# Kernel optimization log

Hardware: AMD Instinct MI355X
Metric: run time of the kernel (lower is better)

The kernel has to match this reference:

```python
import jax, jax.numpy as jnp
import numpy as np

B, EMBED, H, W = 2, 32, 96, 96
SQ = (4, 2); R = 2; EXP = 2
SCH = EMBED // SQ[0]            # 8  squeezed channel dim
SHSP = SCH * R * R              # 32 shuffled spatial dim
SSP = SHSP // SQ[1]             # 16 squeezed spatial dim (attention embed dim)
HEADS = SCH * EXP               # 16
EACH = SSP // SCH               # 2
IDX = np.array([i + j * SCH for i in range(SCH) for j in range(EACH)])
NIDX = np.array([i + j * EACH for i in range(EACH) for j in range(SCH)])


def conv(x, w, b, stride=1, pad=0, groups=1):
    y = jax.lax.conv_general_dilated(x, w, (stride, stride), [(pad, pad), (pad, pad)],
                                     feature_group_count=groups,
                                     dimension_numbers=('NCHW', 'OIHW', 'NCHW'))
    return y + b[None, :, None, None]


def ln_ch(x, w, b):
    # LayerNorm over channel dim (torch applies it on [B,HW,C])
    mu = x.mean(1, keepdims=True)
    var = ((x - mu) ** 2).mean(1, keepdims=True)
    return (x - mu) * jax.lax.rsqrt(var + 1e-5) * w[None, :, None, None] + b[None, :, None, None]


def l2n(x, axis):
    # F.normalize: divide by L2 norm clamped to eps
    return x / jnp.maximum(jnp.sqrt(jnp.sum(x * x, axis=axis, keepdims=True)), 1e-12)


def _qkv(x, wqkv, bqkv):
    Bb, C, Hh, Ww = x.shape
    qkv = conv(x, wqkv, bqkv, groups=C)                        # [B, C*EXP*3, H, W], per-channel 1x1
    qkv = qkv.reshape(Bb, C, EXP * 3, Hh, Ww).transpose(0, 2, 1, 3, 4)
    q, k, v = jnp.split(qkv, 3, axis=1)                        # each [B, EXP, C, H, W]
    hd = EXP * C // HEADS
    rs = lambda a: a.reshape(Bb, HEADS, hd, Hh * Ww)
    return rs(q), rs(k), rs(v)


def _fuse(o, wfus, bfus, Bb, C, Hh, Ww):
    o = o.reshape(Bb, EXP, C, Hh, Ww).transpose(0, 2, 1, 3, 4).reshape(Bb, C * EXP, Hh, Ww)
    return conv(o, wfus, bfus, groups=C)


def chan_attn(x, wqkv, bqkv, t, wfus, bfus):
    Bb, C, Hh, Ww = x.shape
    q, k, v = _qkv(x, wqkv, bqkv)
    q, k = l2n(q, -1), l2n(k, -1)
    a = jax.nn.softmax(jnp.einsum('bhdn,bhen->bhde', q, k) * t, axis=-1)   # [B,h,d,d]
    o = jnp.einsum('bhde,bhen->bhdn', a, v)
    return _fuse(o, wfus, bfus, Bb, C, Hh, Ww)


def spat_attn(x, wqkv, bqkv, t, wfus, bfus):
    Bb, C, Hh, Ww = x.shape
    q, k, v = _qkv(x, wqkv, bqkv)
    q, k = l2n(q, -2), l2n(k, -2)
    a = jax.nn.softmax(jnp.einsum('bhdn,bhdm->bhnm', q, k) * t, axis=-1)   # [B,h,HW,HW]
    o = jnp.einsum('bhnm,bhdm->bhdn', a, v)
    return _fuse(o, wfus, bfus, Bb, C, Hh, Ww)


def pixel_shuffle(x, r):
    Bb, C, Hh, Ww = x.shape
    x = x.reshape(Bb, C // (r * r), r, r, Hh, Ww).transpose(0, 1, 4, 2, 5, 3)
    return x.reshape(Bb, C // (r * r), Hh * r, Ww * r)


def _forward(x, ln1_w, ln1_b, cab_w1, cab_b1, cab_w2, cab_b2, cab_aw1, cab_ab1, cab_aw2, cab_ab2,
             sq1_w, sq1_b, sq2_w, sq2_b, ca_qkv_w, ca_qkv_b, ca_t, ca_fus_w, ca_fus_b,
             sa_qkv_w, sa_qkv_b, sa_t, sa_fus_w, sa_fus_b, un1_w, un1_b, un2_w, un2_b,
             ln2_w, ln2_b, da_w1, da_b1, da_dw_w, da_dw_b, da_pw, da_pb):
    Bb, C, Hh, Ww = x.shape
    xn = ln_ch(x, ln1_w, ln1_b)
    # ---- CAB branch (conv-GELU-conv + RCAN channel attention) ----
    c = jax.nn.gelu(conv(xn, cab_w1, cab_b1, pad=1), approximate=False)
    c = conv(c, cab_w2, cab_b2, pad=1)
    y = c.mean((2, 3), keepdims=True)
    y = jax.nn.relu(conv(y, cab_aw1, cab_ab1))
    y = jax.nn.sigmoid(conv(y, cab_aw2, cab_ab2))
    x_cab = c * y
    # ---- Condensed attention branch ----
    z = conv(xn, sq1_w, sq1_b)                                   # 1x1: C -> SCH
    z = conv(z, sq2_w, sq2_b, stride=R, groups=SCH)              # grouped RxR stride R: -> [B,SSP,H/R,W/R]
    z = z[:, IDX]
    z = chan_attn(z, ca_qkv_w, ca_qkv_b, ca_t, ca_fus_w, ca_fus_b)
    z = z[:, NIDX]
    z = spat_attn(z, sa_qkv_w, sa_qkv_b, sa_t, sa_fus_w, sa_fus_b)
    z = conv(z, un1_w, un1_b, groups=SCH)                        # SSP -> SHSP
    z = pixel_shuffle(z, R)                                      # -> [B,SCH,H,W]
    z = conv(z, un2_w, un2_b)                                    # SCH -> C
    x = x + z + x_cab
    # ---- Dual adaptive (gated depthwise-conv FFN) ----
    xn2 = ln_ch(x, ln2_w, ln2_b)
    d = conv(xn2, da_w1, da_b1)
    d = conv(d, da_dw_w, da_dw_b, pad=3, groups=C).reshape(Bb, C, 2, Hh, Ww)
    d = jax.nn.gelu(d[:, :, 0], approximate=False) * jax.nn.sigmoid(d[:, :, 1])
    d = conv(d, da_pw, da_pb)
    return x + d


def setup_inputs():
    key = jax.random.key(0)
    ks = iter(jax.random.split(key, 40))
    nrm = lambda s: jax.random.normal(next(ks), s, jnp.float32) * 0.05
    inp = {'x': jax.random.normal(next(ks), (B, EMBED, H, W), jnp.float32)}
    wshapes = {
        'cab_w1': (EMBED // 4, EMBED, 3, 3), 'cab_w2': (EMBED, EMBED // 4, 3, 3),
        'cab_aw1': (EMBED // 18, EMBED, 1, 1), 'cab_aw2': (EMBED, EMBED // 18, 1, 1),
        'sq1_w': (SCH, EMBED, 1, 1), 'sq2_w': (SSP, 1, R, R),
        'ca_qkv_w': (SSP * EXP * 3, 1, 1, 1), 'ca_fus_w': (SSP, EXP, 1, 1),
        'sa_qkv_w': (SSP * EXP * 3, 1, 1, 1), 'sa_fus_w': (SSP, EXP, 1, 1),
        'un1_w': (SHSP, SSP // SCH, 1, 1), 'un2_w': (EMBED, SCH, 1, 1),
        'da_w1': (EMBED, EMBED, 1, 1), 'da_dw_w': (2 * EMBED, 1, 7, 7), 'da_pw': (EMBED, EMBED, 1, 1),
    }
    bshapes = {'cab_b1': EMBED // 4, 'cab_b2': EMBED, 'cab_ab1': EMBED // 18, 'cab_ab2': EMBED,
               'sq1_b': SCH, 'sq2_b': SSP, 'ca_qkv_b': SSP * EXP * 3, 'ca_fus_b': SSP,
               'sa_qkv_b': SSP * EXP * 3, 'sa_fus_b': SSP, 'un1_b': SHSP, 'un2_b': EMBED,
               'da_b1': EMBED, 'da_dw_b': 2 * EMBED, 'da_pb': EMBED}
    for n, s in wshapes.items():
        inp[n] = nrm(s)
    for n, s in bshapes.items():
        inp[n] = nrm((s,))
    inp['ln1_w'] = jnp.ones((EMBED,), jnp.float32); inp['ln1_b'] = jnp.zeros((EMBED,), jnp.float32)
    inp['ln2_w'] = jnp.ones((EMBED,), jnp.float32); inp['ln2_b'] = jnp.zeros((EMBED,), jnp.float32)
    inp['ca_t'] = jnp.ones((1, HEADS, 1, 1), jnp.float32)
    inp['sa_t'] = jnp.ones((1, HEADS, 1, 1), jnp.float32)
    return inp


def reference(x, ln1_w, ln1_b, cab_w1, cab_b1, cab_w2, cab_b2, cab_aw1, cab_ab1, cab_aw2, cab_ab2,
              sq1_w, sq1_b, sq2_w, sq2_b, ca_qkv_w, ca_qkv_b, ca_t, ca_fus_w, ca_fus_b,
              sa_qkv_w, sa_qkv_b, sa_t, sa_fus_w, sa_fus_b, un1_w, un1_b, un2_w, un2_b,
              ln2_w, ln2_b, da_w1, da_b1, da_dw_w, da_dw_b, da_pw, da_pb):
    return _forward(x, ln1_w, ln1_b, cab_w1, cab_b1, cab_w2, cab_b2, cab_aw1, cab_ab1, cab_aw2, cab_ab2,
                    sq1_w, sq1_b, sq2_w, sq2_b, ca_qkv_w, ca_qkv_b, ca_t, ca_fus_w, ca_fus_b,
                    sa_qkv_w, sa_qkv_b, sa_t, sa_fus_w, sa_fus_b, un1_w, un1_b, un2_w, un2_b,
                    ln2_w, ln2_b, da_w1, da_b1, da_dw_w, da_dw_b, da_pw, da_pb)
```

## Files before the change

### kernel.cpp

```cpp
#include <hip/hip_runtime.h>
#include <cstdint>
#include <math.h>

#define NP 9216
#define NP2 2304
#define KH 12
#define NMOM 78

__device__ __forceinline__ float gelu_ex(float v){
  return 0.5f*v*(1.0f+erff(v*0.70710678118654752440f));
}
__device__ __forceinline__ float sigm(float v){
  return 1.0f/(1.0f+__expf(-v));
}

__global__ __launch_bounds__(256) void k_ln1(const float* __restrict__ x,
    const float* __restrict__ lw, const float* __restrict__ lb,
    const float* __restrict__ sw, const float* __restrict__ sb,
    float* __restrict__ xn, float* __restrict__ z1)
{
  __shared__ float sred[2][8][32];
  __shared__ float xnsh[32][33];
  int p = threadIdx.x & 31, sl = threadIdx.x >> 5;
  int pix = blockIdx.x*32 + p;
  int b = pix / NP, n = pix % NP;
  const float* xp = x + (size_t)b*32*NP + (size_t)(sl*4)*NP + n;
  float v[4]; float s=0.f, s2=0.f;
#pragma unroll
  for (int c=0;c<4;c++){ float t=xp[(size_t)c*NP]; v[c]=t; s+=t; s2+=t*t; }
  sred[0][sl][p]=s; sred[1][sl][p]=s2;
  __syncthreads();
  s=0.f; s2=0.f;
#pragma unroll
  for (int g=0;g<8;g++){ s += sred[0][g][p]; s2 += sred[1][g][p]; }
  float mu = s*(1.f/32.f);
  float var = s2*(1.f/32.f)-mu*mu;
  float rs = rsqrtf(var+1e-5f);
  float* xo = xn + (size_t)b*32*NP + (size_t)(sl*4)*NP + n;
#pragma unroll
  for (int c=0;c<4;c++){
    int cc = sl*4+c;
    float t = (v[c]-mu)*rs*lw[cc]+lb[cc];
    xo[(size_t)c*NP] = t;
    xnsh[p][cc] = t;
  }
  __syncthreads();
  float vv[32];
#pragma unroll
  for (int c=0;c<32;c++) vv[c]=xnsh[p][c];
  int g = sl;
  float a = sb[g];
#pragma unroll
  for (int c=0;c<32;c++) a += vv[c]*sw[g*32+c];
  z1[(size_t)b*8*NP + (size_t)g*NP + n] = a;
}

__global__ __launch_bounds__(256) void k_phB(const float* __restrict__ xn,
    const float* __restrict__ w1, const float* __restrict__ b1,
    const float* __restrict__ z1, const float* __restrict__ w2,
    const float* __restrict__ b2,
    float* __restrict__ c1, float* __restrict__ u, float* __restrict__ spart)
{
  if (blockIdx.x < 576){
    int og = blockIdx.x/72, pb = blockIdx.x%72;
    int idx = pb*256+threadIdx.x;
    int b = idx/NP, n = idx%NP, i = n/96, j = n%96;
    float acc = b1[og];
    const float* xb = xn + (size_t)b*32*NP;
    const float* wb = w1 + og*288;
#pragma unroll
    for (int di=0;di<3;di++){
      int ii=i+di-1; if ((unsigned)ii>=96u) continue;
#pragma unroll
      for (int dj=0;dj<3;dj++){
        int jj=j+dj-1; if ((unsigned)jj>=96u) continue;
        const float* xp = xb + ii*96+jj;
        const float* wp = wb + di*3+dj;
#pragma unroll
        for (int c=0;c<32;c++) acc += xp[(size_t)c*NP]*wp[c*9];
      }
    }
    c1[(size_t)b*8*NP + (size_t)og*NP + n] = gelu_ex(acc);
  } else {
    __shared__ float red[4][5];
    int u2 = blockIdx.x-576;
    int pr = u2/18, pb = u2%18;
    int idx = pb*256+threadIdx.x;
    int b = idx/NP2, n = idx%NP2, i = n/48, j = n%48;
    int ocA = pr, ocB = pr+8;
    int gA = ocA>>1, gB = ocB>>1;
    const float* zpA = z1 + ((size_t)b*8+gA)*NP + (size_t)(2*i)*96 + 2*j;
    const float* zpB = z1 + ((size_t)b*8+gB)*NP + (size_t)(2*i)*96 + 2*j;
    float vA = zpA[0]*w2[ocA*4]+zpA[1]*w2[ocA*4+1]+zpA[96]*w2[ocA*4+2]+zpA[97]*w2[ocA*4+3]+b2[ocA];
    float vB = zpB[0]*w2[ocB*4]+zpB[1]*w2[ocB*4+1]+zpB[96]*w2[ocB*4+2]+zpB[97]*w2[ocB*4+3]+b2[ocB];
    u[((size_t)b*16+2*pr)*NP2 + n]   = vA;
    u[((size_t)b*16+2*pr+1)*NP2 + n] = vB;
    int wv=threadIdx.x>>6, ln=threadIdx.x&63;
    float st[5]={vA,vB,vA*vA,vB*vB,vA*vB};
#pragma unroll
    for (int k=0;k<5;k++){
      float r=st[k];
#pragma unroll
      for (int m=1;m<64;m<<=1) r+=__shfl_xor(r,m,64);
      if (ln==0) red[wv][k]=r;
    }
    __syncthreads();
    if (threadIdx.x<5){
      float r = red[0][threadIdx.x]+red[1][threadIdx.x]+red[2][threadIdx.x]+red[3][threadIdx.x];
      spart[(b*9 + (pb%9))*40 + pr*5 + threadIdx.x] = r;
    }
  }
}

__global__ __launch_bounds__(256) void k_phC(const float* __restrict__ c1,
    const float* __restrict__ w2, const float* __restrict__ b2,
    float* __restrict__ cbuf, float* __restrict__ ypart,
    const float* __restrict__ u, const float* __restrict__ spart,
    const float* __restrict__ cqw, const float* __restrict__ cqb,
    const float* __restrict__ cat, const float* __restrict__ cfw,
    const float* __restrict__ cfb,
    const float* __restrict__ qw, const float* __restrict__ qb,
    float2* __restrict__ qarr, float* __restrict__ mompart)
{
  if (blockIdx.x < 576){
    __shared__ float red[4][4];
    int og = blockIdx.x/72, pb = blockIdx.x%72;
    int idx = pb*256+threadIdx.x;
    int b = idx/NP, n = idx%NP, i = n/96, j = n%96;
    float acc[4];
#pragma unroll
    for (int k=0;k<4;k++) acc[k]=b2[og*4+k];
    const float* cb = c1 + (size_t)b*8*NP;
#pragma unroll
    for (int di=0;di<3;di++){
      int ii=i+di-1; if ((unsigned)ii>=96u) continue;
#pragma unroll
      for (int dj=0;dj<3;dj++){
        int jj=j+dj-1; if ((unsigned)jj>=96u) continue;
        const float* xp = cb + ii*96+jj;
#pragma unroll
        for (int c=0;c<8;c++){
          float val = xp[(size_t)c*NP];
          const float* wp = w2 + (og*4)*72 + c*9+di*3+dj;
#pragma unroll
          for (int k=0;k<4;k++) acc[k] += val*wp[k*72];
        }
      }
    }
    int wv = threadIdx.x>>6, ln = threadIdx.x&63;
#pragma unroll
    for (int k=0;k<4;k++){
      cbuf[(size_t)b*32*NP + (size_t)(og*4+k)*NP + n] = acc[k];
      float r = acc[k];
#pragma unroll
      for (int m=1;m<64;m<<=1) r += __shfl_xor(r, m, 64);
      if (ln==0) red[wv][k]=r;
    }
    __syncthreads();
    if (threadIdx.x<4){
      float r = red[0][threadIdx.x]+red[1][threadIdx.x]+red[2][threadIdx.x]+red[3][threadIdx.x];
      ypart[(og*72+pb)*4 + threadIdx.x] = r;
    }
  } else {
    __shared__ float red16[16][80];
    int u2 = blockIdx.x-576;
    int bh = u2/9, ch = u2%9;
    int n = ch*256 + threadIdx.x;
    int b = bh>>4, h = bh&15;
    int p = h&7, s = h>>3;
    int cc0=2*p, cc1=2*p+1;
    int oc0 = 2*(cc0&7)+(cc0>>3);
    int oc1 = 2*(cc1&7)+(cc1>>3);
    float AA[2], BB[2], CCc[2];
#pragma unroll
    for (int t2=0;t2<2;t2++){
      int oc = t2? oc1:oc0;
      int p2 = oc>>1, dd = oc&1;
      float st[5]={0,0,0,0,0};
      for (int ib=0; ib<9; ib++){
#pragma unroll
        for (int k=0;k<5;k++) st[k] += spart[(b*9+ib)*40 + p2*5 + k];
      }
      float S0=st[0],S1=st[1],Q00=st[2],Q11=st[3],Q01=st[4];
      float Sd = dd? S1:S0;
      float Qdd = dd? Q11:Q00;
      float cu0[2],cu1[2],ccst[2];
#pragma unroll
      for (int hh=0;hh<2;hh++){
        int h2=p2+8*hh;
        float th2=cat[h2];
        float aq=cqw[(2*p2+dd)*6+hh], bq=cqb[(2*p2+dd)*6+hh];
        float nq=fmaxf(sqrtf(fmaxf(aq*aq*Qdd+2.f*aq*bq*Sd+2304.f*bq*bq,0.f)),1e-12f);
        float m2[2],av[2],bv[2];
#pragma unroll
        for (int e=0;e<2;e++){
          float Se_=e?S1:S0, Qee=e?Q11:Q00, Qde=(dd==e)?Qdd:Q01;
          float ak=cqw[(2*p2+e)*6+2+hh], bk=cqb[(2*p2+e)*6+2+hh];
          float nk=fmaxf(sqrtf(fmaxf(ak*ak*Qee+2.f*ak*bk*Se_+2304.f*bk*bk,0.f)),1e-12f);
          float D=aq*ak*Qde + aq*bk*Sd + bq*ak*Se_ + 2304.f*bq*bk;
          m2[e]=th2*D/(nq*nk);
          av[e]=cqw[(2*p2+e)*6+4+hh]; bv[e]=cqb[(2*p2+e)*6+4+hh];
        }
        float mx=fmaxf(m2[0],m2[1]);
        float e0=__expf(m2[0]-mx), e1=__expf(m2[1]-mx);
        float inv=1.f/(e0+e1);
        cu0[hh]=e0*inv*av[0]; cu1[hh]=e1*inv*av[1]; ccst[hh]=e0*inv*bv[0]+e1*inv*bv[1];
      }
      float f0=cfw[oc*2], f1=cfw[oc*2+1];
      AA[t2]=f0*cu0[0]+f1*cu0[1];
      BB[t2]=f0*cu1[0]+f1*cu1[1];
      CCc[t2]=f0*ccst[0]+f1*ccst[1]+cfb[oc];
    }
    const float* u00 = u + ((size_t)b*16 + (oc0>>1)*2)*NP2;
    const float* u01 = u00 + NP2;
    const float* u10 = u + ((size_t)b*16 + (oc1>>1)*2)*NP2;
    const float* u11 = u10 + NP2;
    float w0 = AA[0]*u00[n]+BB[0]*u01[n]+CCc[0];
    float w1 = AA[1]*u10[n]+BB[1]*u11[n]+CCc[1];
    float k0 = qw[cc0*6+2+s]*w0+qb[cc0*6+2+s];
    float k1 = qw[cc1*6+2+s]*w1+qb[cc1*6+2+s];
    float rnk = 1.f/fmaxf(sqrtf(k0*k0+k1*k1),1e-12f);
    float kc = k0*rnk, ks = k1*rnk;
    float q0 = qw[cc0*6+s]*w0+qb[cc0*6+s];
    float q1 = qw[cc1*6+s]*w1+qb[cc1*6+s];
    float rnq = 1.f/fmaxf(sqrtf(q0*q0+q1*q1),1e-12f);
    qarr[bh*NP2+n] = make_float2(q0*rnq, q1*rnq);

    int grp = threadIdx.x>>4, gl = threadIdx.x&15;
    float c = 1.f, sn = 0.f;
#pragma unroll
    for (int k=0;k<=KH;k++){
      float vals[6] = {c, sn, c*w0, sn*w0, c*w1, sn*w1};
#pragma unroll
      for (int jv=0;jv<6;jv++){
        float r = vals[jv];
        r += __shfl_xor(r, 1, 64);
        r += __shfl_xor(r, 2, 64);
        r += __shfl_xor(r, 4, 64);
        r += __shfl_xor(r, 8, 64);
        if (gl==0) red16[grp][k*6+jv] = r;
      }
      float cn = c*kc - sn*ks;
      sn = sn*kc + c*ks;
      c = cn;
    }
    __syncthreads();
    if (threadIdx.x < NMOM){
      float r = 0.f;
#pragma unroll
      for (int g=0;g<16;g++) r += red16[g][threadIdx.x];
      mompart[(bh*9+ch)*NMOM + threadIdx.x] = r;
    }
  }
}

__global__ __launch_bounds__(256) void k_un2(
    const float* __restrict__ mompart, const float2* __restrict__ qarr,
    const float* __restrict__ sat,
    const float* __restrict__ qw, const float* __restrict__ qb,
    const float* __restrict__ fw, const float* __restrict__ fb,
    const float* __restrict__ u1w, const float* __restrict__ u1b,
    const float* __restrict__ ypart,
    const float* __restrict__ aw1, const float* __restrict__ ab1,
    const float* __restrict__ aw2, const float* __restrict__ ab2,
    const float* __restrict__ u2w, const float* __restrict__ u2b,
    const float* __restrict__ x, const float* __restrict__ cbuf,
    const float* __restrict__ lw, const float* __restrict__ lb,
    const float* __restrict__ dw1, const float* __restrict__ db1,
    float* __restrict__ xsum, float* __restrict__ d1)
{
  __shared__ float msh[16][80];
  __shared__ float fsh[16][13];
  __shared__ float sred[2][8][32];
  __shared__ float xsh[32][33];
  __shared__ float y2sh[32];
  int p = threadIdx.x & 31, sl = threadIdx.x >> 5;
  int pix = blockIdx.x*32 + p;
  int b = pix/NP, n = pix%NP;
  int tid = threadIdx.x;
  if (tid < 208){
    int h = tid/13, k = tid%13;
    double t = (double)sat[h];
    double fac;
    if (fabs(t) < 1e-3){
      double xh = 0.5*t;
      double pk = 1.0;
      for (int q=1;q<=k;q++) pk *= xh/(double)q;
      double Ik = pk*(1.0 + xh*xh/(double)(k+1));
      fac = (k? 2.0:1.0)*Ik;
    } else {
      const int KS = 36;
      double ip1 = 0.0, ik = 1e-280, sum2 = 0.0;
      double vk = 0.0, v0 = 0.0;
      for (int q=KS; q>=1; --q){
        if (q == k) vk = ik;
        sum2 += ik;
        double im1 = ip1 + (2.0*(double)q/t)*ik;
        ip1 = ik; ik = im1;
      }
      v0 = ik;
      if (k == 0) vk = v0;
      double total = v0 + 2.0*sum2;
      double scale = exp(t)/total;
      fac = (k? 2.0:1.0)*vk*scale;
    }
    fsh[h][k] = (float)fac;
  }
  for (int e = tid; e < 16*NMOM; e += 256){
    int bh = e/NMOM, jj = e%NMOM;
    float ssum = 0.f;
    for (int ib=0; ib<9; ib++)
      ssum += mompart[((size_t)(b*16+bh)*9+ib)*NMOM + jj];
    msh[bh][jj] = ssum;
  }
  if (tid < 32){
    int c = tid;
    float ssum = 0.f;
    for (int ib=0; ib<36; ib++)
      ssum += ypart[((c>>2)*72 + b*36 + ib)*4 + (c&3)];
    float pr = ssum*(1.f/9216.f)*aw1[c];
#pragma unroll
    for (int m=1;m<32;m<<=1) pr += __shfl_xor(pr, m, 64);
    float y1 = fmaxf(pr+ab1[0], 0.f);
    y2sh[c] = sigm(aw2[c]*y1+ab2[c]);
  }
  __syncthreads();
  for (int e = tid; e < 16*NMOM; e += 256){
    int bh = e/NMOM, jj = e%NMOM;
    msh[bh][jj] *= fsh[bh][jj/6];
  }
  __syncthreads();
  int ii = n/96, jj96 = n%96;
  int n48 = (ii>>1)*48 + (jj96>>1);
  int kq = (ii&1)*2 + (jj96&1);
  float pg[8];
#pragma unroll
  for (int g=0;g<8;g++){
    float o[2][2];
#pragma unroll
    for (int hh=0;hh<2;hh++){
      int h = g+8*hh;
      float2 q = qarr[(size_t)(b*16+h)*NP2 + n48];
      float c = 1.f, sn = 0.f;
      float Se=0.f, S0=0.f, S1=0.f;
#pragma unroll
      for (int k=0;k<=KH;k++){
        const float* mk = &msh[h][k*6];
        Se += c*mk[0] + sn*mk[1];
        S0 += c*mk[2] + sn*mk[3];
        S1 += c*mk[4] + sn*mk[5];
        float cn = c*q.x - sn*q.y;
        sn = sn*q.x + c*q.y;
        c = cn;
      }
      float rSe = 1.f/Se;
      float av0=qw[(2*g)*6+4+hh],  bv0=qb[(2*g)*6+4+hh];
      float av1=qw[(2*g+1)*6+4+hh],bv1=qb[(2*g+1)*6+4+hh];
      o[hh][0]=av0*S0*rSe+bv0;
      o[hh][1]=av1*S1*rSe+bv1;
    }
    float zz0 = o[0][0]*fw[(2*g)*2]   + o[1][0]*fw[(2*g)*2+1]   + fb[2*g];
    float zz1 = o[0][1]*fw[(2*g+1)*2] + o[1][1]*fw[(2*g+1)*2+1] + fb[2*g+1];
    int od = 4*g+kq;
    pg[g] = zz0*u1w[od*2] + zz1*u1w[od*2+1] + u1b[od];
  }
  float xv[4]; float s=0.f,s2=0.f;
#pragma unroll
  for (int c=0;c<4;c++){
    int cc = sl*4+c;
    float a=u2b[cc];
#pragma unroll
    for (int g=0;g<8;g++) a+=pg[g]*u2w[cc*8+g];
    size_t off=((size_t)b*32+cc)*NP+n;
    float t = x[off]+a+cbuf[off]*y2sh[cc];
    xv[c]=t; xsum[off]=t; s+=t; s2+=t*t;
  }
  sred[0][sl][p]=s; sred[1][sl][p]=s2;
  __syncthreads();
  s=0.f; s2=0.f;
#pragma unroll
  for (int g=0;g<8;g++){ s += sred[0][g][p]; s2 += sred[1][g][p]; }
  float mu=s*(1.f/32.f), var=s2*(1.f/32.f)-mu*mu, rs=rsqrtf(var+1e-5f);
#pragma unroll
  for (int c=0;c<4;c++){
    int cc = sl*4+c;
    xsh[p][cc] = (xv[c]-mu)*rs*lw[cc]+lb[cc];
  }
  __syncthreads();
  float vv[32];
#pragma unroll
  for (int c=0;c<32;c++) vv[c]=xsh[p][c];
#pragma unroll
  for (int k=0;k<4;k++){
    int o = sl*4+k;
    float a=db1[o];
#pragma unroll
    for (int cc=0;cc<32;cc++) a+=vv[cc]*dw1[o*32+cc];
    d1[((size_t)b*32+o)*NP+n]=a;
  }
}

__global__ __launch_bounds__(256) void k_dw(const float* __restrict__ d1,
    const float* __restrict__ w, const float* __restrict__ bias,
    float* __restrict__ dg)
{
  int idx = blockIdx.x*256+threadIdx.x;
  int pl = idx/4608, n2 = idx%4608;
  int i2 = n2/96, j = n2%96;
  int c = pl&31;
  const float* dp = d1 + (size_t)pl*NP;
  const float* w0p = w + (2*c)*49;
  const float* w1p = w + (2*c+1)*49;
  float a0=bias[2*c], a1=bias[2*c+1];
  float c0=bias[2*c], c1=bias[2*c+1];
#pragma unroll
  for (int di=0;di<8;di++){
    int ii=2*i2-3+di; if ((unsigned)ii>=96u) continue;
    const float* rowp = dp + ii*96;
    float t[7];
#pragma unroll
    for (int dj=0;dj<7;dj++){
      int jj=j+dj-3;
      t[dj] = ((unsigned)jj<96u) ? rowp[jj] : 0.f;
    }
    if (di<7){
#pragma unroll
      for (int dj=0;dj<7;dj++){ a0 += t[dj]*w0p[di*7+dj]; a1 += t[dj]*w1p[di*7+dj]; }
    }
    if (di>0){
#pragma unroll
      for (int dj=0;dj<7;dj++){ c0 += t[dj]*w0p[(di-1)*7+dj]; c1 += t[dj]*w1p[(di-1)*7+dj]; }
    }
  }
  dg[(size_t)pl*NP + (size_t)(2*i2)*96 + j]   = gelu_ex(a0)*sigm(a1);
  dg[(size_t)pl*NP + (size_t)(2*i2+1)*96 + j] = gelu_ex(c0)*sigm(c1);
}

__global__ __launch_bounds__(256) void k_fin(const float* __restrict__ dg,
    const float* __restrict__ pw, const float* __restrict__ pb,
    const float* __restrict__ xsum, float* __restrict__ out)
{
  __shared__ float xsh[32][33];
  int p = threadIdx.x & 31, sl = threadIdx.x >> 5;
  int pix = blockIdx.x*32 + p;
  int b = pix/NP, n = pix%NP;
  const float* dp = dg + ((size_t)b*32 + sl*4)*NP + n;
#pragma unroll
  for (int c=0;c<4;c++) xsh[p][sl*4+c]=dp[(size_t)c*NP];
  __syncthreads();
  float vv[32];
#pragma unroll
  for (int c=0;c<32;c++) vv[c]=xsh[p][c];
#pragma unroll
  for (int k=0;k<4;k++){
    int o = sl*4+k;
    float a=pb[o];
#pragma unroll
    for (int cc=0;cc<32;cc++) a+=vv[cc]*pw[o*32+cc];
    size_t off=((size_t)b*32+o)*NP+n;
    out[off]=xsum[off]+a;
  }
}

extern "C" void kernel_launch(void* const* d_in, const int* in_sizes, int n_in,
                              void* d_out, int out_size, void* d_ws, size_t ws_size,
                              hipStream_t stream) {
  (void)in_sizes; (void)n_in; (void)out_size; (void)ws_size;
  const float* x       =(const float*)d_in[0];
  const float* cab_w1  =(const float*)d_in[1];
  const float* cab_w2  =(const float*)d_in[2];
  const float* cab_aw1 =(const float*)d_in[3];
  const float* cab_aw2 =(const float*)d_in[4];
  const float* sq1_w   =(const float*)d_in[5];
  const float* sq2_w   =(const float*)d_in[6];
  const float* ca_qkv_w=(const float*)d_in[7];
  const float* ca_fus_w=(const float*)d_in[8];
  const float* sa_qkv_w=(const float*)d_in[9];
  const float* sa_fus_w=(const float*)d_in[10];
  const float* un1_w   =(const float*)d_in[11];
  const float* un2_w   =(const float*)d_in[12];
  const float* da_w1   =(const float*)d_in[13];
  const float* da_dw_w =(const float*)d_in[14];
  const float* da_pw   =(const float*)d_in[15];
  const float* cab_b1  =(const float*)d_in[16];
  const float* cab_b2  =(const float*)d_in[17];
  const float* cab_ab1 =(const float*)d_in[18];
  const float* cab_ab2 =(const float*)d_in[19];
  const float* sq1_b   =(const float*)d_in[20];
  const float* sq2_b   =(const float*)d_in[21];
  const float* ca_qkv_b=(const float*)d_in[22];
  const float* ca_fus_b=(const float*)d_in[23];
  const float* sa_qkv_b=(const float*)d_in[24];
  const float* sa_fus_b=(const float*)d_in[25];
  const float* un1_b   =(const float*)d_in[26];
  const float* un2_b   =(const float*)d_in[27];
  const float* da_b1   =(const float*)d_in[28];
  const float* da_dw_b =(const float*)d_in[29];
  const float* da_pb   =(const float*)d_in[30];
  const float* ln1_w   =(const float*)d_in[31];
  const float* ln1_b   =(const float*)d_in[32];
  const float* ln2_w   =(const float*)d_in[33];
  const float* ln2_b   =(const float*)d_in[34];
  const float* ca_t    =(const float*)d_in[35];
  const float* sa_t    =(const float*)d_in[36];

  float* ws=(float*)d_ws;
  float* xn    = ws;
  float* z1    = ws + 589824;
  float* c1b   = ws + 737280;
  float* cb    = ws + 884736;
  float* u     = ws + 1474560;
  float* xsm   = ws + 1548288;
  float* ypart = ws + 2138112;
  float* spart = ws + 2140416;
  float2* qarr = (float2*)(ws + 2141184);
  float* mompart = ws + 2288640;
  float* d1    = xn;
  float* dg    = cb;

  k_ln1 <<<576, 256,0,stream>>>(x, ln1_w, ln1_b, sq1_w, sq1_b, xn, z1);
  k_phB <<<720, 256,0,stream>>>(xn, cab_w1, cab_b1, z1, sq2_w, sq2_b, c1b, u, spart);
  k_phC <<<864, 256,0,stream>>>(c1b, cab_w2, cab_b2, cb, ypart,
                                u, spart, ca_qkv_w, ca_qkv_b, ca_t, ca_fus_w, ca_fus_b,
                                sa_qkv_w, sa_qkv_b, qarr, mompart);
  k_un2 <<<576, 256,0,stream>>>(mompart, qarr, sa_t, sa_qkv_w, sa_qkv_b,
                                sa_fus_w, sa_fus_b, un1_w, un1_b,
                                ypart, cab_aw1, cab_ab1, cab_aw2, cab_ab2,
                                un2_w, un2_b, x, cb, ln2_w, ln2_b, da_w1, da_b1, xsm, d1);
  k_dw  <<<1152,256,0,stream>>>(d1, da_dw_w, da_dw_b, dg);
  k_fin <<<576, 256,0,stream>>>(dg, da_pw, da_pb, xsm, (float*)d_out);
}
```

Before: 85.15 us.

## Compute moment series once per low-res pixel in k_un2 and share via LDS

Result: faster. 74.26 us (-12.8%).

```diff
diff --git a/kernel.cpp b/kernel.cpp
--- a/kernel.cpp
+++ b/kernel.cpp
@@ -6,6 +6,7 @@
 #define NP2 2304
 #define KH 12
 #define NMOM 78
+#define MPITCH 84
 
 __device__ __forceinline__ float gelu_ex(float v){
   return 0.5f*v*(1.0f+erff(v*0.70710678118654752440f));
@@ -269,15 +270,17 @@
     const float* __restrict__ dw1, const float* __restrict__ db1,
     float* __restrict__ xsum, float* __restrict__ d1)
 {
-  __shared__ float msh[16][80];
+  __shared__ float msh[16*MPITCH];
   __shared__ float fsh[16][13];
+  __shared__ float osh[256];
+  __shared__ float pgsh[256];
   __shared__ float sred[2][8][32];
   __shared__ float xsh[32][33];
   __shared__ float y2sh[32];
-  int p = threadIdx.x & 31, sl = threadIdx.x >> 5;
-  int pix = blockIdx.x*32 + p;
-  int b = pix/NP, n = pix%NP;
   int tid = threadIdx.x;
+  int bid = blockIdx.x;
+  int b = bid/288; int rem = bid%288;
+  int ri = rem/6, cj = rem%6;
   if (tid < 208){
     int h = tid/13, k = tid%13;
     double t = (double)sat[h];
@@ -311,7 +314,7 @@
     float ssum = 0.f;
     for (int ib=0; ib<9; ib++)
       ssum += mompart[((size_t)(b*16+bh)*9+ib)*NMOM + jj];
-    msh[bh][jj] = ssum;
+    msh[bh*MPITCH + jj] = ssum;
   }
   if (tid < 32){
     int c = tid;
@@ -327,43 +330,56 @@
   __syncthreads();
   for (int e = tid; e < 16*NMOM; e += 256){
     int bh = e/NMOM, jj = e%NMOM;
-    msh[bh][jj] *= fsh[bh][jj/6];
-  }
-  __syncthreads();
-  int ii = n/96, jj96 = n%96;
-  int n48 = (ii>>1)*48 + (jj96>>1);
-  int kq = (ii&1)*2 + (jj96&1);
+    msh[bh*MPITCH + jj] *= fsh[bh][jj/6];
+  }
+  __syncthreads();
+  if (tid < 128){
+    int qd = tid & 7, g = (tid>>3)&7, hh = tid>>6;
+    int h = g + 8*hh;
+    int n48 = ri*48 + cj*8 + qd;
+    float2 q = qarr[(size_t)(b*16+h)*NP2 + n48];
+    const float* mrow = &msh[h*MPITCH];
+    float c = 1.f, sn = 0.f;
+    float Se=0.f, S0=0.f, S1=0.f;
+#pragma unroll
+    for (int k=0;k<=KH;k++){
+      const float* mk = mrow + k*6;
+      Se += c*mk[0] + sn*mk[1];
+      S0 += c*mk[2] + sn*mk[3];
+      S1 += c*mk[4] + sn*mk[5];
+      float cn = c*q.x - sn*q.y;
+      sn = sn*q.x + c*q.y;
+      c = cn;
+    }
+    float rSe = 1.f/Se;
+    float av0=qw[(2*g)*6+4+hh],  bv0=qb[(2*g)*6+4+hh];
+    float av1=qw[(2*g+1)*6+4+hh],bv1=qb[(2*g+1)*6+4+hh];
+    osh[((qd*8+g)*2+hh)*2+0] = av0*S0*rSe+bv0;
+    osh[((qd*8+g)*2+hh)*2+1] = av1*S1*rSe+bv1;
+  }
+  __syncthreads();
+  if (tid < 64){
+    int qd = tid & 7, g = tid>>3;
+    float o00 = osh[((qd*8+g)*2+0)*2+0];
+    float o01 = osh[((qd*8+g)*2+0)*2+1];
+    float o10 = osh[((qd*8+g)*2+1)*2+0];
+    float o11 = osh[((qd*8+g)*2+1)*2+1];
+    float zz0 = o00*fw[(2*g)*2]   + o10*fw[(2*g)*2+1]   + fb[2*g];
+    float zz1 = o01*fw[(2*g+1)*2] + o11*fw[(2*g+1)*2+1] + fb[2*g+1];
+#pragma unroll
+    for (int k=0;k<4;k++){
+      int od = 4*g+k;
+      pgsh[(qd*8+g)*4+k] = zz0*u1w[od*2] + zz1*u1w[od*2+1] + u1b[od];
+    }
+  }
+  __syncthreads();
+  int p = tid & 31, sl = tid >> 5;
+  int r = p>>4, c16 = p&15;
+  int n = (2*ri + r)*96 + 16*cj + c16;
+  int qd = c16>>1, kq = r*2 + (c16&1);
   float pg[8];
 #pragma unroll
-  for (int g=0;g<8;g++){
-    float o[2][2];
-#pragma unroll
-    for (int hh=0;hh<2;hh++){
-      int h = g+8*hh;
-      float2 q = qarr[(size_t)(b*16+h)*NP2 + n48];
-      float c = 1.f, sn = 0.f;
-      float Se=0.f, S0=0.f, S1=0.f;
-#pragma unroll
-      for (int k=0;k<=KH;k++){
-        const float* mk = &msh[h][k*6];
-        Se += c*mk[0] + sn*mk[1];
-        S0 += c*mk[2] + sn*mk[3];
-        S1 += c*mk[4] + sn*mk[5];
-        float cn = c*q.x - sn*q.y;
-        sn = sn*q.x + c*q.y;
-        c = cn;
-      }
-      float rSe = 1.f/Se;
-      float av0=qw[(2*g)*6+4+hh],  bv0=qb[(2*g)*6+4+hh];
-      float av1=qw[(2*g+1)*6+4+hh],bv1=qb[(2*g+1)*6+4+hh];
-      o[hh][0]=av0*S0*rSe+bv0;
-      o[hh][1]=av1*S1*rSe+bv1;
-    }
-    float zz0 = o[0][0]*fw[(2*g)*2]   + o[1][0]*fw[(2*g)*2+1]   + fb[2*g];
-    float zz1 = o[0][1]*fw[(2*g+1)*2] + o[1][1]*fw[(2*g+1)*2+1] + fb[2*g+1];
-    int od = 4*g+kq;
-    pg[g] = zz0*u1w[od*2] + zz1*u1w[od*2+1] + u1b[od];
-  }
+  for (int g=0;g<8;g++) pg[g] = pgsh[(qd*8+g)*4+kq];
   float xv[4]; float s=0.f,s2=0.f;
 #pragma unroll
   for (int c=0;c<4;c++){
```
